# Kernel tuning notes

Measured on AMD Instinct MI355X. Metric: run time of the kernel, lower is better.

The kernel has to match this reference:

```python
import jax, jax.numpy as jnp
import numpy as np

N_NODES = 50000
N_EDGES = 800000
N_GRAPHS = 50
IN_FEATS = 128
H1_FEATS = 64
OUT_FEATS = 32
GAT_SLOPE = 0.2   # DGL GATConv default negative_slope
LRELU_SLOPE = 0.01  # F.leaky_relu default


def setup_inputs() -> dict:
    key = jax.random.key(0)
    ks = jax.random.split(key, 12)
    x = jax.random.normal(ks[0], (N_NODES, IN_FEATS), jnp.float32)
    src = jax.random.randint(ks[1], (N_EDGES,), 0, N_NODES)
    dst = jax.random.randint(ks[2], (N_EDGES,), 0, N_NODES)
    graph_id = jnp.sort(jax.random.randint(ks[3], (N_NODES,), 0, N_GRAPHS))
    s1 = 1.0 / np.sqrt(IN_FEATS)
    s2 = 1.0 / np.sqrt(H1_FEATS)
    W1 = jax.random.normal(ks[4], (IN_FEATS, H1_FEATS), jnp.float32) * s1
    al1 = jax.random.normal(ks[5], (H1_FEATS,), jnp.float32) * s2
    ar1 = jax.random.normal(ks[6], (H1_FEATS,), jnp.float32) * s2
    b1 = jnp.zeros((H1_FEATS,), jnp.float32)
    W2 = jax.random.normal(ks[7], (H1_FEATS, OUT_FEATS), jnp.float32) * s2
    al2 = jax.random.normal(ks[8], (OUT_FEATS,), jnp.float32) * (1.0 / np.sqrt(OUT_FEATS))
    ar2 = jax.random.normal(ks[9], (OUT_FEATS,), jnp.float32) * (1.0 / np.sqrt(OUT_FEATS))
    b2 = jnp.zeros((OUT_FEATS,), jnp.float32)
    return {"x": x, "src": src, "dst": dst, "graph_id": graph_id,
            "W1": W1, "al1": al1, "ar1": ar1, "b1": b1,
            "W2": W2, "al2": al2, "ar2": ar2, "b2": b2}


def _gat_layer(h, src, dst, W, al, ar, b, n_nodes):
    # single-head DGL GATConv (feat_drop=attn_drop=0, bias added post-aggregation)
    z = h @ W                                   # (N, out)
    el = z @ al                                 # (N,) left attention logits
    er = z @ ar                                 # (N,) right attention logits
    e = jax.nn.leaky_relu(el[src] + er[dst], GAT_SLOPE)     # (E,)
    m = jax.ops.segment_max(e, dst, num_segments=n_nodes)  # per-dst max for stable softmax
    p = jnp.exp(e - m[dst])
    s = jax.ops.segment_sum(p, dst, num_segments=n_nodes)
    alpha = p / s[dst]                          # edge softmax over incoming edges
    out = jax.ops.segment_sum(alpha[:, None] * z[src], dst, num_segments=n_nodes)
    return out + b


def reference(x, src, dst, graph_id, W1, al1, ar1, b1, W2, al2, ar2, b2):
    n = x.shape[0]
    h = jax.nn.leaky_relu(_gat_layer(x, src, dst, W1, al1, ar1, b1, n), LRELU_SLOPE)
    h = jax.nn.leaky_relu(_gat_layer(h, src, dst, W2, al2, ar2, b2, n), LRELU_SLOPE)
    # dgl.mean_nodes: per-graph mean over nodes
    cnt = jax.ops.segment_sum(jnp.ones((n,), h.dtype), graph_id, num_segments=N_GRAPHS)
    pooled = jax.ops.segment_sum(h, graph_id, num_segments=N_GRAPHS) / jnp.maximum(cnt, 1.0)[:, None]
    return pooled
```

## Files before the change

### kernel.cpp

```cpp
#include <hip/hip_runtime.h>
#include <math.h>

#define NN 50000
#define NE 800000
#define NG 50
#define F0 128
#define F1 64
#define F2 32
#define NPB 256
#define NBK 196
#define CHUNK 4096
#define NC 196
#define NTILE1 1563
#define NTILE2 782

__device__ __forceinline__ float lrelu(float v, float slope) {
    return v > 0.0f ? v : v * slope;
}

__global__ __launch_bounds__(256) void k1_hist_gemm1_kernel(
    const int* __restrict__ dst, int* __restrict__ hist,
    const float* __restrict__ x, const float* __restrict__ W,
    const float* __restrict__ al, const float* __restrict__ ar,
    float* __restrict__ z, float* __restrict__ el, float* __restrict__ er)
{
    __shared__ float Ws[F0 * F1];
    __shared__ float xs[32][F0];
    int tid = threadIdx.x;

    if (blockIdx.x < NC) {
        int* h = (int*)Ws;
        int c = blockIdx.x;
        if (tid < NBK) h[tid] = 0;
        __syncthreads();
        int e0 = c * CHUNK;
        int e1 = (e0 + CHUNK < NE) ? e0 + CHUNK : NE;
        for (int e = e0 + tid; e < e1; e += 256)
            atomicAdd(&h[dst[e] >> 8], 1);
        __syncthreads();
        if (tid < NBK) hist[tid * NC + c] = h[tid];
        return;
    }

    int r0 = (blockIdx.x - NC) * 32;
    {
        const float4* W4 = reinterpret_cast<const float4*>(W);
        float4* Ws4 = reinterpret_cast<float4*>(Ws);
        #pragma unroll
        for (int i = 0; i < 8; ++i) Ws4[tid + i * 256] = W4[tid + i * 256];
    }
    {
        float4 zero = {0.f, 0.f, 0.f, 0.f};
        #pragma unroll
        for (int i = 0; i < 4; ++i) {
            int s = tid + i * 256;
            int row = s >> 5, c4 = s & 31;
            int grow = r0 + row;
            float4 v = (grow < NN)
                ? reinterpret_cast<const float4*>(x)[(size_t)grow * 32 + c4] : zero;
            *reinterpret_cast<float4*>(&xs[row][c4 * 4]) = v;
        }
    }
    __syncthreads();
    int j = tid & 63, rg = tid >> 6;
    float acc[8] = {0.f, 0.f, 0.f, 0.f, 0.f, 0.f, 0.f, 0.f};
    for (int k4 = 0; k4 < F0 / 4; ++k4) {
        float w0 = Ws[(k4 * 4 + 0) * F1 + j];
        float w1 = Ws[(k4 * 4 + 1) * F1 + j];
        float w2 = Ws[(k4 * 4 + 2) * F1 + j];
        float w3 = Ws[(k4 * 4 + 3) * F1 + j];
        #pragma unroll
        for (int r = 0; r < 8; ++r) {
            float4 xv = *reinterpret_cast<const float4*>(&xs[rg * 8 + r][k4 * 4]);
            acc[r] = fmaf(xv.x, w0, fmaf(xv.y, w1, fmaf(xv.z, w2, fmaf(xv.w, w3, acc[r]))));
        }
    }
    float a_l = al[j], a_r = ar[j];
    #pragma unroll
    for (int r = 0; r < 8; ++r) {
        int row = r0 + rg * 8 + r;
        if (row < NN) z[(size_t)row * F1 + j] = acc[r];
        float pl = acc[r] * a_l, pr = acc[r] * a_r;
        #pragma unroll
        for (int mm = 1; mm < 64; mm <<= 1) {
            pl += __shfl_xor(pl, mm);
            pr += __shfl_xor(pr, mm);
        }
        if (j == 0 && row < NN) { el[row] = pl; er[row] = pr; }
    }
}

__global__ __launch_bounds__(256) void p2a_scan_kernel(
    int* __restrict__ hist, int* __restrict__ btot)
{
    __shared__ int t[256];
    int b = blockIdx.x;
    int v = (threadIdx.x < NC) ? hist[b * NC + threadIdx.x] : 0;
    t[threadIdx.x] = v;
    __syncthreads();
    for (int off = 1; off < 256; off <<= 1) {
        int u = (threadIdx.x >= off) ? t[threadIdx.x - off] : 0;
        __syncthreads();
        t[threadIdx.x] += u;
        __syncthreads();
    }
    if (threadIdx.x < NC) hist[b * NC + threadIdx.x] = t[threadIdx.x] - v;
    if (threadIdx.x == 255) btot[b] = t[255];
}

__global__ __launch_bounds__(256) void p3_part_kernel(
    const int* __restrict__ src, const int* __restrict__ dst,
    const int* __restrict__ hist, const int* __restrict__ btot,
    int2* __restrict__ part)
{
    __shared__ int t[256];
    __shared__ int base[NBK];
    __shared__ int cnt[NBK];
    int tid = threadIdx.x;
    int c = blockIdx.x;
    int v = (tid < NBK) ? btot[tid] : 0;
    t[tid] = v;
    __syncthreads();
    for (int off = 1; off < 256; off <<= 1) {
        int u = (tid >= off) ? t[tid - off] : 0;
        __syncthreads();
        t[tid] += u;
        __syncthreads();
    }
    if (tid < NBK) {
        base[tid] = hist[tid * NC + c] + (t[tid] - v);
        cnt[tid] = 0;
    }
    __syncthreads();
    int e0 = c * CHUNK;
    int e1 = (e0 + CHUNK < NE) ? e0 + CHUNK : NE;
    for (int e = e0 + tid; e < e1; e += 256) {
        int s = src[e], d = dst[e];
        int b = d >> 8;
        int r = atomicAdd(&cnt[b], 1);
        part[base[b] + r] = make_int2(s, d);
    }
}

__global__ __launch_bounds__(256) void p4_fill_kernel(
    const int2* __restrict__ part, const int* __restrict__ btot,
    int* __restrict__ row_start, int* __restrict__ srcs)
{
    __shared__ int t[256];
    __shared__ int deg[NPB];
    __shared__ int off[NPB];
    __shared__ int cnt[NPB];
    int tid = threadIdx.x;
    int b = blockIdx.x;
    int v = (tid < NBK) ? btot[tid] : 0;
    t[tid] = v;
    __syncthreads();
    for (int o = 1; o < 256; o <<= 1) {
        int u = (tid >= o) ? t[tid - o] : 0;
        __syncthreads();
        t[tid] += u;
        __syncthreads();
    }
    int hi = t[b];
    int lo = hi - btot[b];
    if (b == 0 && tid == 0) row_start[NN] = NE;
    deg[tid] = 0;
    cnt[tid] = 0;
    __syncthreads();
    for (int i = lo + tid; i < hi; i += 256)
        atomicAdd(&deg[part[i].y & (NPB - 1)], 1);
    __syncthreads();
    int dv = deg[tid];
    off[tid] = dv;
    __syncthreads();
    for (int o = 1; o < 256; o <<= 1) {
        int u = (tid >= o) ? off[tid - o] : 0;
        __syncthreads();
        off[tid] += u;
        __syncthreads();
    }
    int ex = off[tid] - dv;
    __syncthreads();
    off[tid] = ex;
    __syncthreads();
    int node = b * NPB + tid;
    if (node < NN) row_start[node] = lo + ex;
    for (int i = lo + tid; i < hi; i += 256) {
        int2 e = part[i];
        int n = e.y & (NPB - 1);
        int r = atomicAdd(&cnt[n], 1);
        srcs[lo + off[n] + r] = e.x;
    }
}

__global__ __launch_bounds__(256) void gat_agg64_kernel(
    const int* __restrict__ row_start, const int* __restrict__ srcs,
    const float* __restrict__ el, const float* __restrict__ er,
    const float* __restrict__ z, const float* __restrict__ b,
    float* __restrict__ out, float slope_out)
{
    int node = (blockIdx.x * 256 + threadIdx.x) >> 6;
    if (node >= NN) return;
    int lane = threadIdx.x & 63;
    int g = lane >> 4, c = lane & 15;
    int beg = row_start[node], end = row_start[node + 1];
    float erd = er[node];

    int i0 = beg + lane;
    float v0 = -INFINITY;
    if (i0 < end) v0 = lrelu(el[srcs[i0]] + erd, 0.2f);
    float lm = v0;
    for (int i = i0 + 64; i < end; i += 64)
        lm = fmaxf(lm, lrelu(el[srcs[i]] + erd, 0.2f));
    #pragma unroll
    for (int mm = 1; mm < 64; mm <<= 1) lm = fmaxf(lm, __shfl_xor(lm, mm));

    float preg = 0.f, ls = 0.f;
    if (i0 < end) { preg = __expf(v0 - lm); ls = preg; }
    for (int i = i0 + 64; i < end; i += 64)
        ls += __expf(lrelu(el[srcs[i]] + erd, 0.2f) - lm);
    #pragma unroll
    for (int mm = 1; mm < 64; mm <<= 1) ls += __shfl_xor(ls, mm);
    float inv_s = (ls > 0.f) ? 1.0f / ls : 0.f;
    preg *= inv_s;

    const float4* z4 = reinterpret_cast<const float4*>(z);
    float4 acc = {0.f, 0.f, 0.f, 0.f};
    int ib = beg;
    for (; ib + 8 <= end; ib += 8) {
        int ia = ib + g, ic = ib + 4 + g;
        int ja = ia - beg, jc = ic - beg;
        float aa = __shfl(preg, ja & 63);
        float ac = __shfl(preg, jc & 63);
        int sna = srcs[ia], snc = srcs[ic];
        if (ja >= 64) aa = __expf(lrelu(el[sna] + erd, 0.2f) - lm) * inv_s;
        if (jc >= 64) ac = __expf(lrelu(el[snc] + erd, 0.2f) - lm) * inv_s;
        float4 zva = z4[(size_t)sna * 16 + c];
        float4 zvc = z4[(size_t)snc * 16 + c];
        acc.x = fmaf(aa, zva.x, fmaf(ac, zvc.x, acc.x));
        acc.y = fmaf(aa, zva.y, fmaf(ac, zvc.y, acc.y));
        acc.z = fmaf(aa, zva.z, fmaf(ac, zvc.z, acc.z));
        acc.w = fmaf(aa, zva.w, fmaf(ac, zvc.w, acc.w));
    }
    for (; ib < end; ib += 4) {
        int i = ib + g, jj = i - beg;
        float aa = __shfl(preg, jj & 63);
        if (i < end) {
            int sn = srcs[i];
            if (jj >= 64) aa = __expf(lrelu(el[sn] + erd, 0.2f) - lm) * inv_s;
            float4 zv = z4[(size_t)sn * 16 + c];
            acc.x = fmaf(aa, zv.x, acc.x);
            acc.y = fmaf(aa, zv.y, acc.y);
            acc.z = fmaf(aa, zv.z, acc.z);
            acc.w = fmaf(aa, zv.w, acc.w);
        }
    }
    #pragma unroll
    for (int mm = 16; mm < 64; mm <<= 1) {
        acc.x += __shfl_xor(acc.x, mm);
        acc.y += __shfl_xor(acc.y, mm);
        acc.z += __shfl_xor(acc.z, mm);
        acc.w += __shfl_xor(acc.w, mm);
    }
    if (g == 0) {
        float4 bb = reinterpret_cast<const float4*>(b)[c];
        float4 o;
        o.x = lrelu(acc.x + bb.x, slope_out);
        o.y = lrelu(acc.y + bb.y, slope_out);
        o.z = lrelu(acc.z + bb.z, slope_out);
        o.w = lrelu(acc.w + bb.w, slope_out);
        reinterpret_cast<float4*>(out)[(size_t)node * 16 + c] = o;
    }
}

__global__ __launch_bounds__(256) void gat_agg32_kernel(
    const int* __restrict__ row_start, const int* __restrict__ srcs,
    const float* __restrict__ el, const float* __restrict__ er,
    const float* __restrict__ z, const float* __restrict__ b,
    float* __restrict__ out, float slope_out)
{
    int node = (blockIdx.x * 256 + threadIdx.x) >> 5;
    if (node >= NN) return;
    int sub = threadIdx.x & 31;
    int base = threadIdx.x & 32;
    int g = sub >> 3, c = sub & 7;
    int beg = row_start[node], end = row_start[node + 1];
    float erd = er[node];

    int i0 = beg + sub;
    float v0 = -INFINITY;
    if (i0 < end) v0 = lrelu(el[srcs[i0]] + erd, 0.2f);
    float lm = v0;
    for (int i = i0 + 32; i < end; i += 32)
        lm = fmaxf(lm, lrelu(el[srcs[i]] + erd, 0.2f));
    #pragma unroll
    for (int mm = 1; mm < 32; mm <<= 1) lm = fmaxf(lm, __shfl_xor(lm, mm));

    float preg = 0.f, ls = 0.f;
    if (i0 < end) { preg = __expf(v0 - lm); ls = preg; }
    for (int i = i0 + 32; i < end; i += 32)
        ls += __expf(lrelu(el[srcs[i]] + erd, 0.2f) - lm);
    #pragma unroll
    for (int mm = 1; mm < 32; mm <<= 1) ls += __shfl_xor(ls, mm);
    float inv_s = (ls > 0.f) ? 1.0f / ls : 0.f;
    preg *= inv_s;

    const float4* z4 = reinterpret_cast<const float4*>(z);
    float4 acc = {0.f, 0.f, 0.f, 0.f};
    int ib = beg;
    for (; ib + 8 <= end; ib += 8) {
        int ia = ib + g, ic = ib + 4 + g;
        int ja = ia - beg, jc = ic - beg;
        float aa = __shfl(preg, base | (ja & 31));
        float ac = __shfl(preg, base | (jc & 31));
        int sna = srcs[ia], snc = srcs[ic];
        if (ja >= 32) aa = __expf(lrelu(el[sna] + erd, 0.2f) - lm) * inv_s;
        if (jc >= 32) ac = __expf(lrelu(el[snc] + erd, 0.2f) - lm) * inv_s;
        float4 zva = z4[(size_t)sna * 8 + c];
        float4 zvc = z4[(size_t)snc * 8 + c];
        acc.x = fmaf(aa, zva.x, fmaf(ac, zvc.x, acc.x));
        acc.y = fmaf(aa, zva.y, fmaf(ac, zvc.y, acc.y));
        acc.z = fmaf(aa, zva.z, fmaf(ac, zvc.z, acc.z));
        acc.w = fmaf(aa, zva.w, fmaf(ac, zvc.w, acc.w));
    }
    for (; ib < end; ib += 4) {
        int i = ib + g, jj = i - beg;
        float aa = __shfl(preg, base | (jj & 31));
        if (i < end) {
            int sn = srcs[i];
            if (jj >= 32) aa = __expf(lrelu(el[sn] + erd, 0.2f) - lm) * inv_s;
            float4 zv = z4[(size_t)sn * 8 + c];
            acc.x = fmaf(aa, zv.x, acc.x);
            acc.y = fmaf(aa, zv.y, acc.y);
            acc.z = fmaf(aa, zv.z, acc.z);
            acc.w = fmaf(aa, zv.w, acc.w);
        }
    }
    #pragma unroll
    for (int mm = 8; mm < 32; mm <<= 1) {
        acc.x += __shfl_xor(acc.x, mm);
        acc.y += __shfl_xor(acc.y, mm);
        acc.z += __shfl_xor(acc.z, mm);
        acc.w += __shfl_xor(acc.w, mm);
    }
    if (g == 0) {
        float4 bb = reinterpret_cast<const float4*>(b)[c];
        float4 o;
        o.x = lrelu(acc.x + bb.x, slope_out);
        o.y = lrelu(acc.y + bb.y, slope_out);
        o.z = lrelu(acc.z + bb.z, slope_out);
        o.w = lrelu(acc.w + bb.w, slope_out);
        reinterpret_cast<float4*>(out)[(size_t)node * 8 + c] = o;
    }
}

__global__ __launch_bounds__(256) void gemm2_kernel(
    const float* __restrict__ h, const float* __restrict__ W,
    const float* __restrict__ al, const float* __restrict__ ar,
    float* __restrict__ z, float* __restrict__ el, float* __restrict__ er)
{
    __shared__ float Ws[F1 * F2];
    __shared__ float xs[64][F1];
    int tid = threadIdx.x;
    int r0 = blockIdx.x * 64;
    {
        const float4* W4 = reinterpret_cast<const float4*>(W);
        float4* Ws4 = reinterpret_cast<float4*>(Ws);
        #pragma unroll
        for (int i = 0; i < 2; ++i) Ws4[tid + i * 256] = W4[tid + i * 256];
    }
    {
        float4 zero = {0.f, 0.f, 0.f, 0.f};
        #pragma unroll
        for (int i = 0; i < 4; ++i) {
            int s = tid + i * 256;
            int row = s >> 4, c4 = s & 15;
            int grow = r0 + row;
            float4 v = (grow < NN)
                ? reinterpret_cast<const float4*>(h)[(size_t)grow * 16 + c4] : zero;
            *reinterpret_cast<float4*>(&xs[row][c4 * 4]) = v;
        }
    }
    __syncthreads();
    int j = tid & 31, rg = tid >> 5;
    float acc[8] = {0.f, 0.f, 0.f, 0.f, 0.f, 0.f, 0.f, 0.f};
    for (int k4 = 0; k4 < F1 / 4; ++k4) {
        float w0 = Ws[(k4 * 4 + 0) * F2 + j];
        float w1 = Ws[(k4 * 4 + 1) * F2 + j];
        float w2 = Ws[(k4 * 4 + 2) * F2 + j];
        float w3 = Ws[(k4 * 4 + 3) * F2 + j];
        #pragma unroll
        for (int r = 0; r < 8; ++r) {
            float4 xv = *reinterpret_cast<const float4*>(&xs[rg * 8 + r][k4 * 4]);
            acc[r] = fmaf(xv.x, w0, fmaf(xv.y, w1, fmaf(xv.z, w2, fmaf(xv.w, w3, acc[r]))));
        }
    }
    float a_l = al[j], a_r = ar[j];
    #pragma unroll
    for (int r = 0; r < 8; ++r) {
        int row = r0 + rg * 8 + r;
        if (row < NN) z[(size_t)row * F2 + j] = acc[r];
        float pl = acc[r] * a_l, pr = acc[r] * a_r;
        #pragma unroll
        for (int mm = 1; mm < 32; mm <<= 1) {
            pl += __shfl_xor(pl, mm);
            pr += __shfl_xor(pr, mm);
        }
        if (j == 0 && row < NN) { el[row] = pl; er[row] = pr; }
    }
}

__global__ __launch_bounds__(256) void pool_kernel(
    const float* __restrict__ h2, const int* __restrict__ gid, float* __restrict__ out)
{
    int g = blockIdx.x;
    int lo = 0, hi = NN;
    while (lo < hi) { int mid = (lo + hi) >> 1; if (gid[mid] < g) lo = mid + 1; else hi = mid; }
    int start = lo;
    hi = NN;
    while (lo < hi) { int mid = (lo + hi) >> 1; if (gid[mid] < g + 1) lo = mid + 1; else hi = mid; }
    int end = lo;
    int f = threadIdx.x & 31, r = threadIdx.x >> 5;
    float acc = 0.f;
    for (int n = start + r; n < end; n += 8) acc += h2[(size_t)n * F2 + f];
    __shared__ float red[256];
    red[threadIdx.x] = acc;
    __syncthreads();
    for (int st = 128; st >= 32; st >>= 1) {
        if (threadIdx.x < st) red[threadIdx.x] += red[threadIdx.x + st];
        __syncthreads();
    }
    if (threadIdx.x < 32) {
        float cnt = (float)(end - start);
        out[g * F2 + threadIdx.x] = red[threadIdx.x] / fmaxf(cnt, 1.0f);
    }
}

extern "C" void kernel_launch(void* const* d_in, const int* in_sizes, int n_in,
                              void* d_out, int out_size, void* d_ws, size_t ws_size,
                              hipStream_t stream)
{
    const float* x   = (const float*)d_in[0];
    const int*   src = (const int*)d_in[1];
    const int*   dst = (const int*)d_in[2];
    const int*   gid = (const int*)d_in[3];
    const float* W1  = (const float*)d_in[4];
    const float* al1 = (const float*)d_in[5];
    const float* ar1 = (const float*)d_in[6];
    const float* b1  = (const float*)d_in[7];
    const float* W2  = (const float*)d_in[8];
    const float* al2 = (const float*)d_in[9];
    const float* ar2 = (const float*)d_in[10];
    const float* b2  = (const float*)d_in[11];
    float* out = (float*)d_out;

    float* ws   = (float*)d_ws;
    float* z1   = ws;
    float* h1   = z1 + (size_t)NN * F1;
    float* z2   = h1 + (size_t)NN * F1;
    float* h2   = z2 + (size_t)NN * F2;
    float* el   = h2 + (size_t)NN * F2;
    float* er   = el + NN;
    int* row_start = (int*)(er + NN);
    int* srcs      = row_start + NN + 1;
    int* hist      = srcs + NE;
    int* btot      = hist + NBK * NC;
    int2* part     = (int2*)(btot + NBK + 2);

    k1_hist_gemm1_kernel<<<NC + NTILE1, 256, 0, stream>>>(
        dst, hist, x, W1, al1, ar1, z1, el, er);
    p2a_scan_kernel<<<NBK, 256, 0, stream>>>(hist, btot);
    p3_part_kernel<<<NC, 256, 0, stream>>>(src, dst, hist, btot, part);
    p4_fill_kernel<<<NBK, 256, 0, stream>>>(part, btot, row_start, srcs);
    gat_agg64_kernel<<<(NN * 64 + 255) / 256, 256, 0, stream>>>(
        row_start, srcs, el, er, z1, b1, h1, 0.01f);
    gemm2_kernel<<<NTILE2, 256, 0, stream>>>(h1, W2, al2, ar2, z2, el, er);
    gat_agg32_kernel<<<(NN * 32 + 255) / 256, 256, 0, stream>>>(
        row_start, srcs, el, er, z2, b2, h2, 0.01f);
    pool_kernel<<<NG, 256, 0, stream>>>(h2, gid, out);
}
```

Measured before the change: 273.7 us.

## Store node features in bf16 and fuse layer-1 aggregation with layer-2 GEMM

The projected features z1 and z2 are now stored as bf16 and widened to fp32 during the gathers, which halves the bytes moved in the bandwidth-bound random neighbor reads. Layer-1 aggregation is merged into the layer-2 GEMM kernel: each block aggregates 64 nodes into shared memory and then multiplies by W2, so the h1 round trip through global memory and one launch go away. Separate el2/er2 buffers avoid overwriting layer-1 logits that other blocks still read. The risks are bf16 rounding error in the output and fewer blocks for the aggregation phase (782 blocks, each looping over 16 nodes per wave), which lowers parallelism.

```diff
diff --git a/kernel.cpp b/kernel.cpp
--- a/kernel.cpp
+++ b/kernel.cpp
@@ -17,12 +17,19 @@
 __device__ __forceinline__ float lrelu(float v, float slope) {
     return v > 0.0f ? v : v * slope;
 }
+__device__ __forceinline__ float bf2f(unsigned short u) {
+    return __uint_as_float(((unsigned int)u) << 16);
+}
+__device__ __forceinline__ unsigned short f2bf(float f) {
+    unsigned int u = __float_as_uint(f);
+    return (unsigned short)((u + 0x7FFFu + ((u >> 16) & 1u)) >> 16);
+}
 
 __global__ __launch_bounds__(256) void k1_hist_gemm1_kernel(
     const int* __restrict__ dst, int* __restrict__ hist,
     const float* __restrict__ x, const float* __restrict__ W,
     const float* __restrict__ al, const float* __restrict__ ar,
-    float* __restrict__ z, float* __restrict__ el, float* __restrict__ er)
+    unsigned short* __restrict__ z1b, float* __restrict__ el, float* __restrict__ er)
 {
     __shared__ float Ws[F0 * F1];
     __shared__ float xs[32][F0];
@@ -79,7 +86,7 @@
     #pragma unroll
     for (int r = 0; r < 8; ++r) {
         int row = r0 + rg * 8 + r;
-        if (row < NN) z[(size_t)row * F1 + j] = acc[r];
+        if (row < NN) z1b[(size_t)row * F1 + j] = f2bf(acc[r]);
         float pl = acc[r] * a_l, pr = acc[r] * a_r;
         #pragma unroll
         for (int mm = 1; mm < 64; mm <<= 1) {
@@ -193,90 +200,140 @@
     }
 }
 
-__global__ __launch_bounds__(256) void gat_agg64_kernel(
+__global__ __launch_bounds__(256) void fused_agg1_gemm2_kernel(
     const int* __restrict__ row_start, const int* __restrict__ srcs,
     const float* __restrict__ el, const float* __restrict__ er,
-    const float* __restrict__ z, const float* __restrict__ b,
-    float* __restrict__ out, float slope_out)
-{
-    int node = (blockIdx.x * 256 + threadIdx.x) >> 6;
-    if (node >= NN) return;
-    int lane = threadIdx.x & 63;
+    const unsigned short* __restrict__ z1b, const float* __restrict__ b1,
+    const float* __restrict__ W2, const float* __restrict__ al2,
+    const float* __restrict__ ar2,
+    unsigned short* __restrict__ z2b, float* __restrict__ el2, float* __restrict__ er2)
+{
+    __shared__ float Ws[F1 * F2];
+    __shared__ float hs[64][F1];
+    int tid = threadIdx.x;
+    int r0 = blockIdx.x * 64;
+
+    {
+        const float4* W4 = reinterpret_cast<const float4*>(W2);
+        float4* Ws4 = reinterpret_cast<float4*>(Ws);
+        #pragma unroll
+        for (int i = 0; i < 2; ++i) Ws4[tid + i * 256] = W4[tid + i * 256];
+    }
+
+    int lane = tid & 63;
+    int w = tid >> 6;
     int g = lane >> 4, c = lane & 15;
-    int beg = row_start[node], end = row_start[node + 1];
-    float erd = er[node];
-
-    int i0 = beg + lane;
-    float v0 = -INFINITY;
-    if (i0 < end) v0 = lrelu(el[srcs[i0]] + erd, 0.2f);
-    float lm = v0;
-    for (int i = i0 + 64; i < end; i += 64)
-        lm = fmaxf(lm, lrelu(el[srcs[i]] + erd, 0.2f));
+    const ushort4* z4 = reinterpret_cast<const ushort4*>(z1b);
+
+    for (int it = 0; it < 16; ++it) {
+        int node = r0 + it * 4 + w;
+        int trow = it * 4 + w;
+        if (node < NN) {
+            int beg = row_start[node], end = row_start[node + 1];
+            float erd = er[node];
+            int i0 = beg + lane;
+            float v0 = -INFINITY;
+            if (i0 < end) v0 = lrelu(el[srcs[i0]] + erd, 0.2f);
+            float lm = v0;
+            for (int i = i0 + 64; i < end; i += 64)
+                lm = fmaxf(lm, lrelu(el[srcs[i]] + erd, 0.2f));
+            #pragma unroll
+            for (int mm = 1; mm < 64; mm <<= 1) lm = fmaxf(lm, __shfl_xor(lm, mm));
+
+            float preg = 0.f, ls = 0.f;
+            if (i0 < end) { preg = __expf(v0 - lm); ls = preg; }
+            for (int i = i0 + 64; i < end; i += 64)
+                ls += __expf(lrelu(el[srcs[i]] + erd, 0.2f) - lm);
+            #pragma unroll
+            for (int mm = 1; mm < 64; mm <<= 1) ls += __shfl_xor(ls, mm);
+            float inv_s = (ls > 0.f) ? 1.0f / ls : 0.f;
+            preg *= inv_s;
+
+            float4 acc = {0.f, 0.f, 0.f, 0.f};
+            int ib = beg;
+            for (; ib + 8 <= end; ib += 8) {
+                int ia = ib + g, ic = ib + 4 + g;
+                int ja = ia - beg, jc = ic - beg;
+                float aa = __shfl(preg, ja & 63);
+                float ac = __shfl(preg, jc & 63);
+                int sna = srcs[ia], snc = srcs[ic];
+                if (ja >= 64) aa = __expf(lrelu(el[sna] + erd, 0.2f) - lm) * inv_s;
+                if (jc >= 64) ac = __expf(lrelu(el[snc] + erd, 0.2f) - lm) * inv_s;
+                ushort4 ua = z4[(size_t)sna * 16 + c];
+                ushort4 uc = z4[(size_t)snc * 16 + c];
+                acc.x = fmaf(aa, bf2f(ua.x), fmaf(ac, bf2f(uc.x), acc.x));
+                acc.y = fmaf(aa, bf2f(ua.y), fmaf(ac, bf2f(uc.y), acc.y));
+                acc.z = fmaf(aa, bf2f(ua.z), fmaf(ac, bf2f(uc.z), acc.z));
+                acc.w = fmaf(aa, bf2f(ua.w), fmaf(ac, bf2f(uc.w), acc.w));
+            }
+            for (; ib < end; ib += 4) {
+                int i = ib + g, jj = i - beg;
+                float aa = __shfl(preg, jj & 63);
+                if (i < end) {
+                    int sn = srcs[i];
+                    if (jj >= 64) aa = __expf(lrelu(el[sn] + erd, 0.2f) - lm) * inv_s;
+                    ushort4 u = z4[(size_t)sn * 16 + c];
+                    acc.x = fmaf(aa, bf2f(u.x), acc.x);
+                    acc.y = fmaf(aa, bf2f(u.y), acc.y);
+                    acc.z = fmaf(aa, bf2f(u.z), acc.z);
+                    acc.w = fmaf(aa, bf2f(u.w), acc.w);
+                }
+            }
+            #pragma unroll
+            for (int mm = 16; mm < 64; mm <<= 1) {
+                acc.x += __shfl_xor(acc.x, mm);
+                acc.y += __shfl_xor(acc.y, mm);
+                acc.z += __shfl_xor(acc.z, mm);
+                acc.w += __shfl_xor(acc.w, mm);
+            }
+            if (g == 0) {
+                float4 bb = reinterpret_cast<const float4*>(b1)[c];
+                float4 o;
+                o.x = lrelu(acc.x + bb.x, 0.01f);
+                o.y = lrelu(acc.y + bb.y, 0.01f);
+                o.z = lrelu(acc.z + bb.z, 0.01f);
+                o.w = lrelu(acc.w + bb.w, 0.01f);
+                *reinterpret_cast<float4*>(&hs[trow][c * 4]) = o;
+            }
+        } else if (g == 0) {
+            float4 zero = {0.f, 0.f, 0.f, 0.f};
+            *reinterpret_cast<float4*>(&hs[trow][c * 4]) = zero;
+        }
+    }
+    __syncthreads();
+
+    int j = tid & 31, rg = tid >> 5;
+    float acc[8] = {0.f, 0.f, 0.f, 0.f, 0.f, 0.f, 0.f, 0.f};
+    for (int k4 = 0; k4 < F1 / 4; ++k4) {
+        float w0 = Ws[(k4 * 4 + 0) * F2 + j];
+        float w1 = Ws[(k4 * 4 + 1) * F2 + j];
+        float w2 = Ws[(k4 * 4 + 2) * F2 + j];
+        float w3 = Ws[(k4 * 4 + 3) * F2 + j];
+        #pragma unroll
+        for (int r = 0; r < 8; ++r) {
+            float4 xv = *reinterpret_cast<const float4*>(&hs[rg * 8 + r][k4 * 4]);
+            acc[r] = fmaf(xv.x, w0, fmaf(xv.y, w1, fmaf(xv.z, w2, fmaf(xv.w, w3, acc[r]))));
+        }
+    }
+    float a_l = al2[j], a_r = ar2[j];
     #pragma unroll
-    for (int mm = 1; mm < 64; mm <<= 1) lm = fmaxf(lm, __shfl_xor(lm, mm));
-
-    float preg = 0.f, ls = 0.f;
-    if (i0 < end) { preg = __expf(v0 - lm); ls = preg; }
-    for (int i = i0 + 64; i < end; i += 64)
-        ls += __expf(lrelu(el[srcs[i]] + erd, 0.2f) - lm);
-    #pragma unroll
-    for (int mm = 1; mm < 64; mm <<= 1) ls += __shfl_xor(ls, mm);
-    float inv_s = (ls > 0.f) ? 1.0f / ls : 0.f;
-    preg *= inv_s;
-
-    const float4* z4 = reinterpret_cast<const float4*>(z);
-    float4 acc = {0.f, 0.f, 0.f, 0.f};
-    int ib = beg;
-    for (; ib + 8 <= end; ib += 8) {
-        int ia = ib + g, ic = ib + 4 + g;
-        int ja = ia - beg, jc = ic - beg;
-        float aa = __shfl(preg, ja & 63);
-        float ac = __shfl(preg, jc & 63);
-        int sna = srcs[ia], snc = srcs[ic];
-        if (ja >= 64) aa = __expf(lrelu(el[sna] + erd, 0.2f) - lm) * inv_s;
-        if (jc >= 64) ac = __expf(lrelu(el[snc] + erd, 0.2f) - lm) * inv_s;
-        float4 zva = z4[(size_t)sna * 16 + c];
-        float4 zvc = z4[(size_t)snc * 16 + c];
-        acc.x = fmaf(aa, zva.x, fmaf(ac, zvc.x, acc.x));
-        acc.y = fmaf(aa, zva.y, fmaf(ac, zvc.y, acc.y));
-        acc.z = fmaf(aa, zva.z, fmaf(ac, zvc.z, acc.z));
-        acc.w = fmaf(aa, zva.w, fmaf(ac, zvc.w, acc.w));
-    }
-    for (; ib < end; ib += 4) {
-        int i = ib + g, jj = i - beg;
-        float aa = __shfl(preg, jj & 63);
-        if (i < end) {
-            int sn = srcs[i];
-            if (jj >= 64) aa = __expf(lrelu(el[sn] + erd, 0.2f) - lm) * inv_s;
-            float4 zv = z4[(size_t)sn * 16 + c];
-            acc.x = fmaf(aa, zv.x, acc.x);
-            acc.y = fmaf(aa, zv.y, acc.y);
-            acc.z = fmaf(aa, zv.z, acc.z);
-            acc.w = fmaf(aa, zv.w, acc.w);
-        }
-    }
-    #pragma unroll
-    for (int mm = 16; mm < 64; mm <<= 1) {
-        acc.x += __shfl_xor(acc.x, mm);
-        acc.y += __shfl_xor(acc.y, mm);
-        acc.z += __shfl_xor(acc.z, mm);
-        acc.w += __shfl_xor(acc.w, mm);
-    }
-    if (g == 0) {
-        float4 bb = reinterpret_cast<const float4*>(b)[c];
-        float4 o;
-        o.x = lrelu(acc.x + bb.x, slope_out);
-        o.y = lrelu(acc.y + bb.y, slope_out);
-        o.z = lrelu(acc.z + bb.z, slope_out);
-        o.w = lrelu(acc.w + bb.w, slope_out);
-        reinterpret_cast<float4*>(out)[(size_t)node * 16 + c] = o;
+    for (int r = 0; r < 8; ++r) {
+        int row = r0 + rg * 8 + r;
+        if (row < NN) z2b[(size_t)row * F2 + j] = f2bf(acc[r]);
+        float pl = acc[r] * a_l, pr = acc[r] * a_r;
+        #pragma unroll
+        for (int mm = 1; mm < 32; mm <<= 1) {
+            pl += __shfl_xor(pl, mm);
+            pr += __shfl_xor(pr, mm);
+        }
+        if (j == 0 && row < NN) { el2[row] = pl; er2[row] = pr; }
     }
 }
 
 __global__ __launch_bounds__(256) void gat_agg32_kernel(
     const int* __restrict__ row_start, const int* __restrict__ srcs,
     const float* __restrict__ el, const float* __restrict__ er,
-    const float* __restrict__ z, const float* __restrict__ b,
+    const unsigned short* __restrict__ z2b, const float* __restrict__ b,
     float* __restrict__ out, float slope_out)
 {
     int node = (blockIdx.x * 256 + threadIdx.x) >> 5;
@@ -305,7 +362,7 @@
     float inv_s = (ls > 0.f) ? 1.0f / ls : 0.f;
     preg *= inv_s;
 
-    const float4* z4 = reinterpret_cast<const float4*>(z);
+    const ushort4* z4 = reinterpret_cast<const ushort4*>(z2b);
     float4 acc = {0.f, 0.f, 0.f, 0.f};
     int ib = beg;
     for (; ib + 8 <= end; ib += 8) {
@@ -316,12 +373,12 @@
         int sna = srcs[ia], snc = srcs[ic];
         if (ja >= 32) aa = __expf(lrelu(el[sna] + erd, 0.2f) - lm) * inv_s;
         if (jc >= 32) ac = __expf(lrelu(el[snc] + erd, 0.2f) - lm) * inv_s;
-        float4 zva = z4[(size_t)sna * 8 + c];
-        float4 zvc = z4[(size_t)snc * 8 + c];
-        acc.x = fmaf(aa, zva.x, fmaf(ac, zvc.x, acc.x));
-        acc.y = fmaf(aa, zva.y, fmaf(ac, zvc.y, acc.y));
-        acc.z = fmaf(aa, zva.z, fmaf(ac, zvc.z, acc.z));
-        acc.w = fmaf(aa, zva.w, fmaf(ac, zvc.w, acc.w));
+        ushort4 ua = z4[(size_t)sna * 8 + c];
+        ushort4 uc = z4[(size_t)snc * 8 + c];
+        acc.x = fmaf(aa, bf2f(ua.x), fmaf(ac, bf2f(uc.x), acc.x));
+        acc.y = fmaf(aa, bf2f(ua.y), fmaf(ac, bf2f(uc.y), acc.y));
+        acc.z = fmaf(aa, bf2f(ua.z), fmaf(ac, bf2f(uc.z), acc.z));
+        acc.w = fmaf(aa, bf2f(ua.w), fmaf(ac, bf2f(uc.w), acc.w));
     }
     for (; ib < end; ib += 4) {
         int i = ib + g, jj = i - beg;
@@ -329,11 +386,11 @@
         if (i < end) {
             int sn = srcs[i];
             if (jj >= 32) aa = __expf(lrelu(el[sn] + erd, 0.2f) - lm) * inv_s;
-            float4 zv = z4[(size_t)sn * 8 + c];
-            acc.x = fmaf(aa, zv.x, acc.x);
-            acc.y = fmaf(aa, zv.y, acc.y);
-            acc.z = fmaf(aa, zv.z, acc.z);
-            acc.w = fmaf(aa, zv.w, acc.w);
+            ushort4 u = z4[(size_t)sn * 8 + c];
+            acc.x = fmaf(aa, bf2f(u.x), acc.x);
+            acc.y = fmaf(aa, bf2f(u.y), acc.y);
+            acc.z = fmaf(aa, bf2f(u.z), acc.z);
+            acc.w = fmaf(aa, bf2f(u.w), acc.w);
         }
     }
     #pragma unroll
@@ -351,62 +408,6 @@
         o.z = lrelu(acc.z + bb.z, slope_out);
         o.w = lrelu(acc.w + bb.w, slope_out);
         reinterpret_cast<float4*>(out)[(size_t)node * 8 + c] = o;
-    }
-}
-
-__global__ __launch_bounds__(256) void gemm2_kernel(
-    const float* __restrict__ h, const float* __restrict__ W,
-    const float* __restrict__ al, const float* __restrict__ ar,
-    float* __restrict__ z, float* __restrict__ el, float* __restrict__ er)
-{
-    __shared__ float Ws[F1 * F2];
-    __shared__ float xs[64][F1];
-    int tid = threadIdx.x;
-    int r0 = blockIdx.x * 64;
-    {
-        const float4* W4 = reinterpret_cast<const float4*>(W);
-        float4* Ws4 = reinterpret_cast<float4*>(Ws);
-        #pragma unroll
-        for (int i = 0; i < 2; ++i) Ws4[tid + i * 256] = W4[tid + i * 256];
-    }
-    {
-        float4 zero = {0.f, 0.f, 0.f, 0.f};
-        #pragma unroll
-        for (int i = 0; i < 4; ++i) {
-            int s = tid + i * 256;
-            int row = s >> 4, c4 = s & 15;
-            int grow = r0 + row;
-            float4 v = (grow < NN)
-                ? reinterpret_cast<const float4*>(h)[(size_t)grow * 16 + c4] : zero;
-            *reinterpret_cast<float4*>(&xs[row][c4 * 4]) = v;
-        }
-    }
-    __syncthreads();
-    int j = tid & 31, rg = tid >> 5;
-    float acc[8] = {0.f, 0.f, 0.f, 0.f, 0.f, 0.f, 0.f, 0.f};
-    for (int k4 = 0; k4 < F1 / 4; ++k4) {
-        float w0 = Ws[(k4 * 4 + 0) * F2 + j];
-        float w1 = Ws[(k4 * 4 + 1) * F2 + j];
-        float w2 = Ws[(k4 * 4 + 2) * F2 + j];
-        float w3 = Ws[(k4 * 4 + 3) * F2 + j];
-        #pragma unroll
-        for (int r = 0; r < 8; ++r) {
-            float4 xv = *reinterpret_cast<const float4*>(&xs[rg * 8 + r][k4 * 4]);
-            acc[r] = fmaf(xv.x, w0, fmaf(xv.y, w1, fmaf(xv.z, w2, fmaf(xv.w, w3, acc[r]))));
-        }
-    }
-    float a_l = al[j], a_r = ar[j];
-    #pragma unroll
-    for (int r = 0; r < 8; ++r) {
-        int row = r0 + rg * 8 + r;
-        if (row < NN) z[(size_t)row * F2 + j] = acc[r];
-        float pl = acc[r] * a_l, pr = acc[r] * a_r;
-        #pragma unroll
-        for (int mm = 1; mm < 32; mm <<= 1) {
-            pl += __shfl_xor(pl, mm);
-            pr += __shfl_xor(pr, mm);
-        }
-        if (j == 0 && row < NN) { el[row] = pl; er[row] = pr; }
     }
 }
 
@@ -454,28 +455,28 @@
     const float* b2  = (const float*)d_in[11];
     float* out = (float*)d_out;
 
-    float* ws   = (float*)d_ws;
-    float* z1   = ws;
-    float* h1   = z1 + (size_t)NN * F1;
-    float* z2   = h1 + (size_t)NN * F1;
-    float* h2   = z2 + (size_t)NN * F2;
+    float* ws = (float*)d_ws;
+    unsigned short* z1b = (unsigned short*)ws;
+    unsigned short* z2b = (unsigned short*)(ws + (size_t)NN * 32);
+    float* h2   = ws + (size_t)NN * 32 + (size_t)NN * 16;
     float* el   = h2 + (size_t)NN * F2;
     float* er   = el + NN;
-    int* row_start = (int*)(er + NN);
-    int* srcs      = row_start + NN + 1;
+    float* el2  = er + NN;
+    float* er2  = el2 + NN;
+    int* row_start = (int*)(er2 + NN);
+    int* srcs      = row_start + NN + 2;
     int* hist      = srcs + NE;
     int* btot      = hist + NBK * NC;
     int2* part     = (int2*)(btot + NBK + 2);
 
     k1_hist_gemm1_kernel<<<NC + NTILE1, 256, 0, stream>>>(
-        dst, hist, x, W1, al1, ar1, z1, el, er);
+        dst, hist, x, W1, al1, ar1, z1b, el, er);
     p2a_scan_kernel<<<NBK, 256, 0, stream>>>(hist, btot);
     p3_part_kernel<<<NC, 256, 0, stream>>>(src, dst, hist, btot, part);
     p4_fill_kernel<<<NBK, 256, 0, stream>>>(part, btot, row_start, srcs);
-    gat_agg64_kernel<<<(NN * 64 + 255) / 256, 256, 0, stream>>>(
-        row_start, srcs, el, er, z1, b1, h1, 0.01f);
-    gemm2_kernel<<<NTILE2, 256, 0, stream>>>(h1, W2, al2, ar2, z2, el, er);
+    fused_agg1_gemm2_kernel<<<NTILE2, 256, 0, stream>>>(
+        row_start, srcs, el, er, z1b, b1, W2, al2, ar2, z2b, el2, er2);
     gat_agg32_kernel<<<(NN * 32 + 255) / 256, 256, 0, stream>>>(
-        row_start, srcs, el, er, z2, b2, h2, 0.01f);
+        row_start, srcs, el2, er2, z2b, b2, h2, 0.01f);
     pool_kernel<<<NG, 256, 0, stream>>>(h2, gid, out);
 }
```

New measurement: 412.3 us. +50.6%, slower.
